# Kernel tuning notes

Hardware: AMD Instinct MI355X
Metric: run time of the kernel (lower is better)

The kernel has to match this reference:

```python
import jax, jax.numpy as jnp
import numpy as np

N = 40000      # nodes
E = 640000     # edges
D = 128        # input_dim == hidden_dim
G = 64         # graphs in batch


def _mk_linear(key, din, dout):
    kw, kb = jax.random.split(key)
    w = jax.random.normal(kw, (din, dout), jnp.float32) / np.sqrt(din)
    b = jax.random.normal(kb, (dout,), jnp.float32) * 0.01
    return w, b


def setup_inputs() -> dict:
    key = jax.random.key(0)
    ks = jax.random.split(key, 12)
    x = jax.random.normal(ks[0], (N, D), jnp.float32)
    edge_attr = jax.random.normal(ks[1], (E, D), jnp.float32)
    edge_index = jax.random.randint(ks[2], (2, E), 0, N, jnp.int32)
    batch = jnp.sort(jax.random.randint(ks[3], (N,), 0, G, jnp.int32))
    inp = {"x": x, "edge_attr": edge_attr, "edge_index": edge_index, "batch": batch}
    # 4 GINE layers, each with a 2-layer MLP (Linear-ReLU-Linear)
    for i in range(4):
        w1, b1 = _mk_linear(ks[4 + 2 * i], D, D)
        w2, b2 = _mk_linear(ks[5 + 2 * i], D, D)
        inp[f"w{i+1}_1"] = w1
        inp[f"b{i+1}_1"] = b1
        inp[f"w{i+1}_2"] = w2
        inp[f"b{i+1}_2"] = b2
    return inp


def _gine_layer(x, src, dst, edge_attr, w1, b1, w2, b2):
    # message: ReLU(x_src + edge_attr), scatter-sum into dst (PyG GINEConv, eps=0)
    msg = jax.nn.relu(x[src] + edge_attr)                      # [E, D]
    agg = jax.ops.segment_sum(msg, dst, num_segments=N)       # [N, D]
    h = x + agg                                                # (1+eps)*x + agg, eps=0
    h = jnp.maximum(h @ w1 + b1, 0.0) @ w2 + b2                # 2-layer MLP
    return h


def reference(x, edge_attr, edge_index, batch,
              w1_1, b1_1, w1_2, b1_2,
              w2_1, b2_1, w2_2, b2_2,
              w3_1, b3_1, w3_2, b3_2,
              w4_1, b4_1, w4_2, b4_2):
    src, dst = edge_index[0], edge_index[1]
    h = x
    params = [(w1_1, b1_1, w1_2, b1_2), (w2_1, b2_1, w2_2, b2_2),
              (w3_1, b3_1, w3_2, b3_2), (w4_1, b4_1, w4_2, b4_2)]
    for (w1, b1, w2, b2) in params:
        h = jax.nn.relu(_gine_layer(h, src, dst, edge_attr, w1, b1, w2, b2))
    # global mean pool over graphs
    sums = jax.ops.segment_sum(h, batch, num_segments=G)                 # [G, D]
    cnts = jax.ops.segment_sum(jnp.ones((N,), h.dtype), batch, num_segments=G)
    return sums / jnp.maximum(cnts, 1.0)[:, None]
```

## Files before the change

kernel.cpp:

```cpp
#include <hip/hip_runtime.h>

#define NN 40000
#define NE 640000
#define DD 128
#define NG 64

typedef float vf4 __attribute__((ext_vector_type(4)));
typedef unsigned short us4 __attribute__((ext_vector_type(4)));
typedef unsigned short us8 __attribute__((ext_vector_type(8)));
typedef short bf16x8 __attribute__((ext_vector_type(8)));
typedef float f32x4 __attribute__((ext_vector_type(4)));

__device__ inline unsigned short f2bf(float f) {
    unsigned int u = __float_as_uint(f);
    return (unsigned short)((u + 0x7fffu + ((u >> 16) & 1u)) >> 16);
}
__device__ inline float bf2f(unsigned short s) {
    return __uint_as_float((unsigned int)s << 16);
}

__global__ __launch_bounds__(256) void cvt_k(const float* __restrict__ ea,
                                             unsigned short* __restrict__ eb)
{
    size_t i = ((size_t)blockIdx.x * 256 + threadIdx.x) * 8;
    vf4 a = __builtin_nontemporal_load((const vf4*)(ea + i));
    vf4 b = __builtin_nontemporal_load((const vf4*)(ea + i + 4));
    us4 o0 = {f2bf(a.x), f2bf(a.y), f2bf(a.z), f2bf(a.w)};
    us4 o1 = {f2bf(b.x), f2bf(b.y), f2bf(b.z), f2bf(b.w)};
    *(us4*)(eb + i) = o0;
    *(us4*)(eb + i + 4) = o1;
}

__global__ __launch_bounds__(256) void wcvt_k(
    const float* __restrict__ m0, const float* __restrict__ m1,
    const float* __restrict__ m2, const float* __restrict__ m3,
    const float* __restrict__ m4, const float* __restrict__ m5,
    const float* __restrict__ m6, const float* __restrict__ m7,
    unsigned short* __restrict__ hi, unsigned short* __restrict__ lo)
{
    const float* ms[8] = {m0, m1, m2, m3, m4, m5, m6, m7};
    int mat = blockIdx.x >> 6;
    int idx = (blockIdx.x & 63) * 256 + threadIdx.x;
    float v = ms[mat][idx];
    int k = idx >> 7, n = idx & 127;
    unsigned short h = f2bf(v);
    size_t o = ((size_t)mat << 14) + (size_t)n * DD + k;
    hi[o] = h;
    lo[o] = f2bf(v - bf2f(h));
}

__global__ __launch_bounds__(256) void hist_k(const int* __restrict__ dst,
                                              int* __restrict__ cnt)
{
    int e = blockIdx.x * 256 + threadIdx.x;
    if (e < NE) atomicAdd(&cnt[dst[e]], 1);
}

__global__ __launch_bounds__(1024) void scan_k(const int* __restrict__ cnt,
                                               int* __restrict__ row_ptr,
                                               int* __restrict__ cursor)
{
    __shared__ int sm[1024];
    int t = threadIdx.x;
    int base = t * 40;
    int s = 0;
#pragma unroll 8
    for (int i = 0; i < 40; ++i) {
        int idx = base + i;
        if (idx < NN) s += cnt[idx];
    }
    sm[t] = s;
    __syncthreads();
    for (int off = 1; off < 1024; off <<= 1) {
        int x = (t >= off) ? sm[t - off] : 0;
        __syncthreads();
        sm[t] += x;
        __syncthreads();
    }
    int run = sm[t] - s;
#pragma unroll 8
    for (int i = 0; i < 40; ++i) {
        int idx = base + i;
        if (idx < NN) {
            row_ptr[idx] = run;
            cursor[idx] = run;
            run += cnt[idx];
        }
    }
    if (t == 1023) row_ptr[NN] = run;
}

__global__ __launch_bounds__(256) void fill_k(const int* __restrict__ src,
                                              const int* __restrict__ dst,
                                              int* __restrict__ cursor,
                                              int2* __restrict__ elist)
{
    int e = blockIdx.x * 256 + threadIdx.x;
    if (e < NE) {
        int d = dst[e];
        int pos = atomicAdd(&cursor[d], 1);
        elist[pos] = make_int2(src[e], e);
    }
}

__device__ inline void acc1(float4& acc, const unsigned short* __restrict__ hb,
                            const unsigned short* __restrict__ eb,
                            int s, int id, int lane)
{
    us4 xv = *(const us4*)(hb + (size_t)s * DD + lane * 4);
    us4 bv = *(const us4*)(eb + (size_t)id * DD + lane * 4);
    acc.x += fmaxf(bf2f(xv.x) + bf2f(bv.x), 0.f);
    acc.y += fmaxf(bf2f(xv.y) + bf2f(bv.y), 0.f);
    acc.z += fmaxf(bf2f(xv.z) + bf2f(bv.z), 0.f);
    acc.w += fmaxf(bf2f(xv.w) + bf2f(bv.w), 0.f);
}

__global__ __launch_bounds__(256) void gather_bf(
    const unsigned short* __restrict__ hb, const unsigned short* __restrict__ eb,
    const int* __restrict__ row_ptr, const int2* __restrict__ elist,
    float* __restrict__ agg)
{
    int grp = blockIdx.x * 8 + (threadIdx.x >> 5);
    int lane = threadIdx.x & 31;
    if (grp >= NN) return;
    int beg = row_ptr[grp], end = row_ptr[grp + 1];

    float4 a0 = make_float4(0.f, 0.f, 0.f, 0.f);
    float4 a1 = make_float4(0.f, 0.f, 0.f, 0.f);
    float4 a2 = make_float4(0.f, 0.f, 0.f, 0.f);
    float4 a3 = make_float4(0.f, 0.f, 0.f, 0.f);
    int e = beg;
    for (; e + 4 <= end; e += 4) {
        int2 p0 = elist[e];
        int2 p1 = elist[e + 1];
        int2 p2 = elist[e + 2];
        int2 p3 = elist[e + 3];
        acc1(a0, hb, eb, p0.x, p0.y, lane);
        acc1(a1, hb, eb, p1.x, p1.y, lane);
        acc1(a2, hb, eb, p2.x, p2.y, lane);
        acc1(a3, hb, eb, p3.x, p3.y, lane);
    }
    for (; e < end; ++e) {
        int2 p0 = elist[e];
        acc1(a0, hb, eb, p0.x, p0.y, lane);
    }
    us4 sv = *(const us4*)(hb + (size_t)grp * DD + lane * 4);
    float4 o;
    o.x = bf2f(sv.x) + (a0.x + a1.x) + (a2.x + a3.x);
    o.y = bf2f(sv.y) + (a0.y + a1.y) + (a2.y + a3.y);
    o.z = bf2f(sv.z) + (a0.z + a1.z) + (a2.z + a3.z);
    o.w = bf2f(sv.w) + (a0.w + a1.w) + (a2.w + a3.w);
    *(float4*)(agg + (size_t)grp * DD + lane * 4) = o;
}

__device__ inline void acc1f(float4& acc, const float* __restrict__ h,
                             const float* __restrict__ ea,
                             int s, int id, int lane)
{
    const float4 xv = *(const float4*)(h + (size_t)s * DD + lane * 4);
    vf4 ev = __builtin_nontemporal_load((const vf4*)(ea + (size_t)id * DD + lane * 4));
    acc.x += fmaxf(xv.x + ev.x, 0.f);
    acc.y += fmaxf(xv.y + ev.y, 0.f);
    acc.z += fmaxf(xv.z + ev.z, 0.f);
    acc.w += fmaxf(xv.w + ev.w, 0.f);
}

__global__ __launch_bounds__(256) void gather_f32(
    const float* __restrict__ h, const float* __restrict__ ea,
    const int* __restrict__ row_ptr, const int2* __restrict__ elist,
    float* __restrict__ agg)
{
    int grp = blockIdx.x * 8 + (threadIdx.x >> 5);
    int lane = threadIdx.x & 31;
    if (grp >= NN) return;
    int beg = row_ptr[grp], end = row_ptr[grp + 1];

    float4 a0 = make_float4(0.f, 0.f, 0.f, 0.f);
    float4 a1 = make_float4(0.f, 0.f, 0.f, 0.f);
    float4 a2 = make_float4(0.f, 0.f, 0.f, 0.f);
    float4 a3 = make_float4(0.f, 0.f, 0.f, 0.f);
    int e = beg;
    for (; e + 4 <= end; e += 4) {
        int2 p0 = elist[e];
        int2 p1 = elist[e + 1];
        int2 p2 = elist[e + 2];
        int2 p3 = elist[e + 3];
        acc1f(a0, h, ea, p0.x, p0.y, lane);
        acc1f(a1, h, ea, p1.x, p1.y, lane);
        acc1f(a2, h, ea, p2.x, p2.y, lane);
        acc1f(a3, h, ea, p3.x, p3.y, lane);
    }
    for (; e < end; ++e) {
        int2 p0 = elist[e];
        acc1f(a0, h, ea, p0.x, p0.y, lane);
    }
    const float4 sv = *(const float4*)(h + (size_t)grp * DD + lane * 4);
    float4 o;
    o.x = sv.x + (a0.x + a1.x) + (a2.x + a3.x);
    o.y = sv.y + (a0.y + a1.y) + (a2.y + a3.y);
    o.z = sv.z + (a0.z + a1.z) + (a2.z + a3.z);
    o.w = sv.w + (a0.w + a1.w) + (a2.w + a3.w);
    *(float4*)(agg + (size_t)grp * DD + lane * 4) = o;
}

template <int OUT>
__global__ __launch_bounds__(256) void mfma_mlp(
    const float* A,
    const unsigned short* __restrict__ Wh,
    const unsigned short* __restrict__ Wl,
    const float* __restrict__ bias,
    float* C, unsigned short* Cb)
{
    __shared__ __align__(16) char lds[96 * 1024];
    char* lAh = lds;
    char* lAl = lds + 16 * 1024;
    char* lBh = lds + 32 * 1024;
    char* lBl = lds + 64 * 1024;

    const int tid = threadIdx.x;
    const int m0 = blockIdx.x * 64;

    {
        const int row = tid >> 2;
        const int c0 = (tid & 3) * 32;
        const float* srcp = A + (size_t)(m0 + row) * DD + c0;
        const int base = row * 256 + c0 * 2;
        const int sw = (row & 7) << 4;
#pragma unroll
        for (int i = 0; i < 4; ++i) {
            float4 v0 = *(const float4*)(srcp + i * 8);
            float4 v1 = *(const float4*)(srcp + i * 8 + 4);
            float f[8] = {v0.x, v0.y, v0.z, v0.w, v1.x, v1.y, v1.z, v1.w};
            us8 hv, lv;
#pragma unroll
            for (int j = 0; j < 8; ++j) {
                unsigned short hb = f2bf(f[j]);
                hv[j] = hb;
                lv[j] = f2bf(f[j] - bf2f(hb));
            }
            const int off = (base + i * 16) ^ sw;
            *(us8*)(lAh + off) = hv;
            *(us8*)(lAl + off) = lv;
        }
    }
    {
        const int n = tid >> 1;
        const int k0 = (tid & 1) * 64;
        const unsigned short* sh = Wh + (size_t)n * DD + k0;
        const unsigned short* sl = Wl + (size_t)n * DD + k0;
        const int base = n * 256 + k0 * 2;
        const int sw = (n & 7) << 4;
#pragma unroll
        for (int i = 0; i < 8; ++i) {
            const int off = (base + i * 16) ^ sw;
            *(us8*)(lBh + off) = *(const us8*)(sh + i * 8);
            *(us8*)(lBl + off) = *(const us8*)(sl + i * 8);
        }
    }
    __syncthreads();

    const int lane = tid & 63;
    const int wid = tid >> 6;
    const int lr = lane & 15;
    const int kg = lane >> 4;
    const int swr = (lr & 7) << 4;

    bf16x8 ah[4], al[4];
#pragma unroll
    for (int ks = 0; ks < 4; ++ks) {
        const int off = ((wid * 16 + lr) * 256 + ks * 64 + kg * 16) ^ swr;
        ah[ks] = *(const bf16x8*)(lAh + off);
        al[ks] = *(const bf16x8*)(lAl + off);
    }
    f32x4 acc[8];
#pragma unroll
    for (int nf = 0; nf < 8; ++nf) acc[nf] = (f32x4){0.f, 0.f, 0.f, 0.f};
#pragma unroll
    for (int nf = 0; nf < 8; ++nf) {
#pragma unroll
        for (int ks = 0; ks < 4; ++ks) {
            const int off = ((nf * 16 + lr) * 256 + ks * 64 + kg * 16) ^ swr;
            bf16x8 bh = *(const bf16x8*)(lBh + off);
            bf16x8 bl = *(const bf16x8*)(lBl + off);
            acc[nf] = __builtin_amdgcn_mfma_f32_16x16x32_bf16(ah[ks], bh, acc[nf], 0, 0, 0);
            acc[nf] = __builtin_amdgcn_mfma_f32_16x16x32_bf16(ah[ks], bl, acc[nf], 0, 0, 0);
            acc[nf] = __builtin_amdgcn_mfma_f32_16x16x32_bf16(al[ks], bh, acc[nf], 0, 0, 0);
        }
    }
#pragma unroll
    for (int nf = 0; nf < 8; ++nf) {
        const int col = nf * 16 + lr;
        const float b = bias[col];
        float v[4];
#pragma unroll
        for (int r = 0; r < 4; ++r) v[r] = fmaxf(acc[nf][r] + b, 0.0f);
        const size_t rbase = (size_t)(m0 + wid * 16 + kg * 4) * DD + col;
        if (OUT & 1) {
#pragma unroll
            for (int r = 0; r < 4; ++r) C[rbase + (size_t)r * DD] = v[r];
        }
        if (OUT & 2) {
#pragma unroll
            for (int r = 0; r < 4; ++r) Cb[rbase + (size_t)r * DD] = f2bf(v[r]);
        }
    }
}

__device__ inline void pool_flush(float* __restrict__ out, int g, int lane,
                                  const float4& acc)
{
    float* o = out + (size_t)g * DD + lane * 4;
    unsafeAtomicAdd(o + 0, acc.x);
    unsafeAtomicAdd(o + 1, acc.y);
    unsafeAtomicAdd(o + 2, acc.z);
    unsafeAtomicAdd(o + 3, acc.w);
}

__global__ __launch_bounds__(256) void pool_k(
    const float* __restrict__ h, const int* __restrict__ batch,
    float* __restrict__ out, int* __restrict__ cnt)
{
    int tid = blockIdx.x * 256 + threadIdx.x;
    int grp = tid >> 5;
    int lane = tid & 31;
    int n0 = grp * 16;
    if (n0 >= NN) return;
    int nend = min(n0 + 16, NN);

    float4 acc = make_float4(0.f, 0.f, 0.f, 0.f);
    int gprev = batch[n0];
    int crun = 0;
    for (int n = n0; n < nend; ++n) {
        int g = batch[n];
        if (g != gprev) {
            pool_flush(out, gprev, lane, acc);
            if (lane == 0) atomicAdd(cnt + gprev, crun);
            acc = make_float4(0.f, 0.f, 0.f, 0.f);
            crun = 0;
            gprev = g;
        }
        float4 v = *(const float4*)(h + (size_t)n * DD + lane * 4);
        acc.x += v.x; acc.y += v.y; acc.z += v.z; acc.w += v.w;
        ++crun;
    }
    pool_flush(out, gprev, lane, acc);
    if (lane == 0) atomicAdd(cnt + gprev, crun);
}

__global__ __launch_bounds__(256) void pool_div_k(float* __restrict__ out,
                                                  const int* __restrict__ cnt)
{
    int tid = blockIdx.x * 256 + threadIdx.x;
    if (tid >= NG * DD) return;
    int g = tid / DD;
    float c = fmaxf((float)cnt[g], 1.0f);
    out[tid] = out[tid] / c;
}

extern "C" void kernel_launch(void* const* d_in, const int* in_sizes, int n_in,
                              void* d_out, int out_size, void* d_ws, size_t ws_size,
                              hipStream_t stream)
{
    const float* x     = (const float*)d_in[0];
    const float* ea    = (const float*)d_in[1];
    const int*   ei    = (const int*)d_in[2];
    const int*   batch = (const int*)d_in[3];
    const float* w1[4], * b1[4], * w2[4], * b2[4];
    for (int l = 0; l < 4; ++l) {
        w1[l] = (const float*)d_in[4 + 4 * l];
        b1[l] = (const float*)d_in[5 + 4 * l];
        w2[l] = (const float*)d_in[6 + 4 * l];
        b2[l] = (const float*)d_in[7 + 4 * l];
    }

    const int* srcp = ei;
    const int* dstp = ei + NE;

    char* ws = (char*)d_ws;
    const size_t hbytes = (size_t)NN * DD * sizeof(float);
    float* agg = (float*)ws;
    float* hA  = (float*)(ws + hbytes);
    char*  p   = ws + 2 * hbytes;
    int*  cnt_node = (int*)p;           p += ((NN * 4 + 255) & ~255);
    int*  row_ptr  = (int*)p;           p += (((NN + 1) * 4 + 255) & ~255);
    int*  cursor   = (int*)p;           p += ((NN * 4 + 255) & ~255);
    int2* elist    = (int2*)p;          p += (((size_t)NE * 8 + 255) & ~255);
    int*  cntG     = (int*)p;           p += 256;
    unsigned short* wt_hi = (unsigned short*)p;  p += (size_t)8 * 16384 * 2;
    unsigned short* wt_lo = (unsigned short*)p;  p += (size_t)8 * 16384 * 2;
    unsigned short* hB = (unsigned short*)p;     p += (size_t)NN * DD * 2;
    unsigned short* ea_bf = (unsigned short*)p;
    const size_t need_bf = (size_t)(p - ws) + (size_t)NE * DD * 2;
    const bool use_bf = (ws_size >= need_bf);

    const int eblocks     = (NE + 255) / 256;
    const int gblocks     = (NN + 7) / 8;
    const int gemm_blocks = NN / 64;
    const int pool_blocks = ((NN / 16) * 32 + 255) / 256;

    if (use_bf) {
        cvt_k<<<(size_t)NE * DD / 8 / 256, 256, 0, stream>>>(ea, ea_bf);
        cvt_k<<<(size_t)NN * DD / 8 / 256, 256, 0, stream>>>(x, hB);
    }
    wcvt_k<<<512, 256, 0, stream>>>(w1[0], w2[0], w1[1], w2[1],
                                    w1[2], w2[2], w1[3], w2[3], wt_hi, wt_lo);
    hipMemsetAsync(cnt_node, 0, NN * sizeof(int), stream);
    hist_k<<<eblocks, 256, 0, stream>>>(dstp, cnt_node);
    scan_k<<<1, 1024, 0, stream>>>(cnt_node, row_ptr, cursor);
    fill_k<<<eblocks, 256, 0, stream>>>(srcp, dstp, cursor, elist);

    if (use_bf) {
        for (int l = 0; l < 4; ++l) {
            gather_bf<<<gblocks, 256, 0, stream>>>(hB, ea_bf, row_ptr, elist, agg);
            const unsigned short* h1  = wt_hi + ((size_t)(2 * l) << 14);
            const unsigned short* lo1 = wt_lo + ((size_t)(2 * l) << 14);
            const unsigned short* h2  = wt_hi + ((size_t)(2 * l + 1) << 14);
            const unsigned short* lo2 = wt_lo + ((size_t)(2 * l + 1) << 14);
            mfma_mlp<1><<<gemm_blocks, 256, 0, stream>>>(agg, h1, lo1, b1[l],
                                                         agg, nullptr);
            if (l < 3)
                mfma_mlp<2><<<gemm_blocks, 256, 0, stream>>>(agg, h2, lo2, b2[l],
                                                             nullptr, hB);
            else
                mfma_mlp<1><<<gemm_blocks, 256, 0, stream>>>(agg, h2, lo2, b2[l],
                                                             hA, nullptr);
        }
    } else {
        const float* hcur = x;
        for (int l = 0; l < 4; ++l) {
            gather_f32<<<gblocks, 256, 0, stream>>>(hcur, ea, row_ptr, elist, agg);
            const unsigned short* h1  = wt_hi + ((size_t)(2 * l) << 14);
            const unsigned short* lo1 = wt_lo + ((size_t)(2 * l) << 14);
            const unsigned short* h2  = wt_hi + ((size_t)(2 * l + 1) << 14);
            const unsigned short* lo2 = wt_lo + ((size_t)(2 * l + 1) << 14);
            mfma_mlp<1><<<gemm_blocks, 256, 0, stream>>>(agg, h1, lo1, b1[l],
                                                         agg, nullptr);
            mfma_mlp<1><<<gemm_blocks, 256, 0, stream>>>(agg, h2, lo2, b2[l],
                                                         hA, nullptr);
            hcur = hA;
        }
    }

    hipMemsetAsync(d_out, 0, (size_t)NG * DD * sizeof(float), stream);
    hipMemsetAsync(cntG, 0, NG * sizeof(int), stream);
    pool_k<<<pool_blocks, 256, 0, stream>>>(hA, batch, (float*)d_out, cntG);
    pool_div_k<<<(NG * DD + 255) / 256, 256, 0, stream>>>((float*)d_out, cntG);
}
```

Baseline: 1.027 ms.

## Fuse two MLP GEMMs into one kernel and fold edge_attr conversion into first gather

The two Linear layers of each GINE MLP now run in a single kernel: the hidden activations stay in LDS as hi/lo bf16 splits and the second weight matrix is loaded after a barrier, so the intermediate [N,D] fp32 tensor never goes through global memory. The separate edge_attr fp32-to-bf16 conversion pass is removed; the first-layer gather reads fp32 edge_attr, converts it on the fly and writes the bf16 copy that later layers reuse. This saves one kernel launch per layer and a full read-plus-write pass over edge_attr, at the cost of scattered bf16 writes in the first gather and extra barriers in the MLP kernel.

Result: faster. 1.001 ms (-2.5%).

```diff
diff --git a/kernel.cpp b/kernel.cpp
--- a/kernel.cpp
+++ b/kernel.cpp
@@ -115,8 +115,25 @@
     acc.w += fmaxf(bf2f(xv.w) + bf2f(bv.w), 0.f);
 }
 
+__device__ inline void acc1_cvt(float4& acc, const unsigned short* __restrict__ hb,
+                                const float* __restrict__ ea,
+                                unsigned short* __restrict__ eb,
+                                int s, int id, int lane)
+{
+    us4 xv = *(const us4*)(hb + (size_t)s * DD + lane * 4);
+    const float4 ev = *(const float4*)(ea + (size_t)id * DD + lane * 4);
+    us4 bv = {f2bf(ev.x), f2bf(ev.y), f2bf(ev.z), f2bf(ev.w)};
+    *(us4*)(eb + (size_t)id * DD + lane * 4) = bv;
+    acc.x += fmaxf(bf2f(xv.x) + bf2f(bv.x), 0.f);
+    acc.y += fmaxf(bf2f(xv.y) + bf2f(bv.y), 0.f);
+    acc.z += fmaxf(bf2f(xv.z) + bf2f(bv.z), 0.f);
+    acc.w += fmaxf(bf2f(xv.w) + bf2f(bv.w), 0.f);
+}
+
+template <int L0>
 __global__ __launch_bounds__(256) void gather_bf(
-    const unsigned short* __restrict__ hb, const unsigned short* __restrict__ eb,
+    const unsigned short* __restrict__ hb, const unsigned short* __restrict__ eb_r,
+    const float* __restrict__ ea, unsigned short* __restrict__ eb_w,
     const int* __restrict__ row_ptr, const int2* __restrict__ elist,
     float* __restrict__ agg)
 {
@@ -135,14 +152,22 @@
         int2 p1 = elist[e + 1];
         int2 p2 = elist[e + 2];
         int2 p3 = elist[e + 3];
-        acc1(a0, hb, eb, p0.x, p0.y, lane);
-        acc1(a1, hb, eb, p1.x, p1.y, lane);
-        acc1(a2, hb, eb, p2.x, p2.y, lane);
-        acc1(a3, hb, eb, p3.x, p3.y, lane);
+        if (L0) {
+            acc1_cvt(a0, hb, ea, eb_w, p0.x, p0.y, lane);
+            acc1_cvt(a1, hb, ea, eb_w, p1.x, p1.y, lane);
+            acc1_cvt(a2, hb, ea, eb_w, p2.x, p2.y, lane);
+            acc1_cvt(a3, hb, ea, eb_w, p3.x, p3.y, lane);
+        } else {
+            acc1(a0, hb, eb_r, p0.x, p0.y, lane);
+            acc1(a1, hb, eb_r, p1.x, p1.y, lane);
+            acc1(a2, hb, eb_r, p2.x, p2.y, lane);
+            acc1(a3, hb, eb_r, p3.x, p3.y, lane);
+        }
     }
     for (; e < end; ++e) {
         int2 p0 = elist[e];
-        acc1(a0, hb, eb, p0.x, p0.y, lane);
+        if (L0) acc1_cvt(a0, hb, ea, eb_w, p0.x, p0.y, lane);
+        else    acc1(a0, hb, eb_r, p0.x, p0.y, lane);
     }
     us4 sv = *(const us4*)(hb + (size_t)grp * DD + lane * 4);
     float4 o;
@@ -204,11 +229,12 @@
 }
 
 template <int OUT>
-__global__ __launch_bounds__(256) void mfma_mlp(
-    const float* A,
-    const unsigned short* __restrict__ Wh,
-    const unsigned short* __restrict__ Wl,
-    const float* __restrict__ bias,
+__global__ __launch_bounds__(256) void mlp_fused(
+    const float* __restrict__ A,
+    const unsigned short* __restrict__ W1h, const unsigned short* __restrict__ W1l,
+    const float* __restrict__ b1v,
+    const unsigned short* __restrict__ W2h, const unsigned short* __restrict__ W2l,
+    const float* __restrict__ b2v,
     float* C, unsigned short* Cb)
 {
     __shared__ __align__(16) char lds[96 * 1024];
@@ -243,16 +269,16 @@
             *(us8*)(lAl + off) = lv;
         }
     }
+    const int wn = tid >> 1;
+    const int wk0 = (tid & 1) * 64;
+    const int wbase = wn * 256 + wk0 * 2;
+    const int wsw = (wn & 7) << 4;
     {
-        const int n = tid >> 1;
-        const int k0 = (tid & 1) * 64;
-        const unsigned short* sh = Wh + (size_t)n * DD + k0;
-        const unsigned short* sl = Wl + (size_t)n * DD + k0;
-        const int base = n * 256 + k0 * 2;
-        const int sw = (n & 7) << 4;
+        const unsigned short* sh = W1h + (size_t)wn * DD + wk0;
+        const unsigned short* sl = W1l + (size_t)wn * DD + wk0;
 #pragma unroll
         for (int i = 0; i < 8; ++i) {
-            const int off = (base + i * 16) ^ sw;
+            const int off = (wbase + i * 16) ^ wsw;
             *(us8*)(lBh + off) = *(const us8*)(sh + i * 8);
             *(us8*)(lBl + off) = *(const us8*)(sl + i * 8);
         }
@@ -287,10 +313,58 @@
             acc[nf] = __builtin_amdgcn_mfma_f32_16x16x32_bf16(al[ks], bh, acc[nf], 0, 0, 0);
         }
     }
+    __syncthreads();
+
 #pragma unroll
     for (int nf = 0; nf < 8; ++nf) {
         const int col = nf * 16 + lr;
-        const float b = bias[col];
+        const float b = b1v[col];
+#pragma unroll
+        for (int r = 0; r < 4; ++r) {
+            float u = fmaxf(acc[nf][r] + b, 0.0f);
+            const int lrow = wid * 16 + kg * 4 + r;
+            const int off = (lrow * 256 + col * 2) ^ ((lrow & 7) << 4);
+            unsigned short hb = f2bf(u);
+            *(unsigned short*)(lAh + off) = hb;
+            *(unsigned short*)(lAl + off) = f2bf(u - bf2f(hb));
+        }
+    }
+    {
+        const unsigned short* sh = W2h + (size_t)wn * DD + wk0;
+        const unsigned short* sl = W2l + (size_t)wn * DD + wk0;
+#pragma unroll
+        for (int i = 0; i < 8; ++i) {
+            const int off = (wbase + i * 16) ^ wsw;
+            *(us8*)(lBh + off) = *(const us8*)(sh + i * 8);
+            *(us8*)(lBl + off) = *(const us8*)(sl + i * 8);
+        }
+    }
+    __syncthreads();
+
+#pragma unroll
+    for (int ks = 0; ks < 4; ++ks) {
+        const int off = ((wid * 16 + lr) * 256 + ks * 64 + kg * 16) ^ swr;
+        ah[ks] = *(const bf16x8*)(lAh + off);
+        al[ks] = *(const bf16x8*)(lAl + off);
+    }
+#pragma unroll
+    for (int nf = 0; nf < 8; ++nf) acc[nf] = (f32x4){0.f, 0.f, 0.f, 0.f};
+#pragma unroll
+    for (int nf = 0; nf < 8; ++nf) {
+#pragma unroll
+        for (int ks = 0; ks < 4; ++ks) {
+            const int off = ((nf * 16 + lr) * 256 + ks * 64 + kg * 16) ^ swr;
+            bf16x8 bh = *(const bf16x8*)(lBh + off);
+            bf16x8 bl = *(const bf16x8*)(lBl + off);
+            acc[nf] = __builtin_amdgcn_mfma_f32_16x16x32_bf16(ah[ks], bh, acc[nf], 0, 0, 0);
+            acc[nf] = __builtin_amdgcn_mfma_f32_16x16x32_bf16(ah[ks], bl, acc[nf], 0, 0, 0);
+            acc[nf] = __builtin_amdgcn_mfma_f32_16x16x32_bf16(al[ks], bh, acc[nf], 0, 0, 0);
+        }
+    }
+#pragma unroll
+    for (int nf = 0; nf < 8; ++nf) {
+        const int col = nf * 16 + lr;
+        const float b = b2v[col];
         float v[4];
 #pragma unroll
         for (int r = 0; r < 4; ++r) v[r] = fmaxf(acc[nf][r] + b, 0.0f);
@@ -398,10 +472,8 @@
     const int gemm_blocks = NN / 64;
     const int pool_blocks = ((NN / 16) * 32 + 255) / 256;
 
-    if (use_bf) {
-        cvt_k<<<(size_t)NE * DD / 8 / 256, 256, 0, stream>>>(ea, ea_bf);
+    if (use_bf)
         cvt_k<<<(size_t)NN * DD / 8 / 256, 256, 0, stream>>>(x, hB);
-    }
     wcvt_k<<<512, 256, 0, stream>>>(w1[0], w2[0], w1[1], w2[1],
                                     w1[2], w2[2], w1[3], w2[3], wt_hi, wt_lo);
     hipMemsetAsync(cnt_node, 0, NN * sizeof(int), stream);
@@ -411,19 +483,22 @@
 
     if (use_bf) {
         for (int l = 0; l < 4; ++l) {
-            gather_bf<<<gblocks, 256, 0, stream>>>(hB, ea_bf, row_ptr, elist, agg);
+            if (l == 0)
+                gather_bf<1><<<gblocks, 256, 0, stream>>>(hB, nullptr, ea, ea_bf,
+                                                          row_ptr, elist, agg);
+            else
+                gather_bf<0><<<gblocks, 256, 0, stream>>>(hB, ea_bf, nullptr, nullptr,
+                                                          row_ptr, elist, agg);
             const unsigned short* h1  = wt_hi + ((size_t)(2 * l) << 14);
             const unsigned short* lo1 = wt_lo + ((size_t)(2 * l) << 14);
             const unsigned short* h2  = wt_hi + ((size_t)(2 * l + 1) << 14);
             const unsigned short* lo2 = wt_lo + ((size_t)(2 * l + 1) << 14);
-            mfma_mlp<1><<<gemm_blocks, 256, 0, stream>>>(agg, h1, lo1, b1[l],
-                                                         agg, nullptr);
             if (l < 3)
-                mfma_mlp<2><<<gemm_blocks, 256, 0, stream>>>(agg, h2, lo2, b2[l],
-                                                             nullptr, hB);
+                mlp_fused<2><<<gemm_blocks, 256, 0, stream>>>(
+                    agg, h1, lo1, b1[l], h2, lo2, b2[l], nullptr, hB);
             else
-                mfma_mlp<1><<<gemm_blocks, 256, 0, stream>>>(agg, h2, lo2, b2[l],
-                                                             hA, nullptr);
+                mlp_fused<1><<<gemm_blocks, 256, 0, stream>>>(
+                    agg, h1, lo1, b1[l], h2, lo2, b2[l], hA, nullptr);
         }
     } else {
         const float* hcur = x;
@@ -433,10 +508,8 @@
             const unsigned short* lo1 = wt_lo + ((size_t)(2 * l) << 14);
             const unsigned short* h2  = wt_hi + ((size_t)(2 * l + 1) << 14);
             const unsigned short* lo2 = wt_lo + ((size_t)(2 * l + 1) << 14);
-            mfma_mlp<1><<<gemm_blocks, 256, 0, stream>>>(agg, h1, lo1, b1[l],
-                                                         agg, nullptr);
-            mfma_mlp<1><<<gemm_blocks, 256, 0, stream>>>(agg, h2, lo2, b2[l],
-                                                         hA, nullptr);
+            mlp_fused<1><<<gemm_blocks, 256, 0, stream>>>(
+                agg, h1, lo1, b1[l], h2, lo2, b2[l], hA, nullptr);
             hcur = hA;
         }
     }
```
